# Optimization experiments

Measured on AMD Instinct MI355X. Metric: run time of the kernel, lower is better.

Reference implementation:

```python
import jax, jax.numpy as jnp
import numpy as np

C_CT, C_MRI, C_OUT = 64, 64, 64
B, D, H, W = 1, 8, 32, 32


def setup_inputs() -> dict:
    key = jax.random.key(0)
    ks = jax.random.split(key, 18)
    s = 0.05
    inp = {
        "ct_features": jax.random.normal(ks[0], (B, C_CT, D, H, W), jnp.float32),
        "mri_features": jax.random.normal(ks[1], (B, C_MRI, D, H, W), jnp.float32),
        # 1x1x1 Conv3d == per-voxel linear: weight (out, in), bias (out,)
        "wq_ct": jax.random.normal(ks[2], (C_OUT, C_CT), jnp.float32) * s,
        "bq_ct": jax.random.normal(ks[3], (C_OUT,), jnp.float32) * s,
        "wk_mri": jax.random.normal(ks[4], (C_OUT, C_MRI), jnp.float32) * s,
        "bk_mri": jax.random.normal(ks[5], (C_OUT,), jnp.float32) * s,
        "wv_mri": jax.random.normal(ks[6], (C_OUT, C_MRI), jnp.float32) * s,
        "bv_mri": jax.random.normal(ks[7], (C_OUT,), jnp.float32) * s,
        "wq_mri": jax.random.normal(ks[8], (C_OUT, C_MRI), jnp.float32) * s,
        "bq_mri": jax.random.normal(ks[9], (C_OUT,), jnp.float32) * s,
        "wk_ct": jax.random.normal(ks[10], (C_OUT, C_CT), jnp.float32) * s,
        "bk_ct": jax.random.normal(ks[11], (C_OUT,), jnp.float32) * s,
        "wv_ct": jax.random.normal(ks[12], (C_OUT, C_CT), jnp.float32) * s,
        "bv_ct": jax.random.normal(ks[13], (C_OUT,), jnp.float32) * s,
        "wo": jax.random.normal(ks[14], (C_OUT, 2 * C_OUT), jnp.float32) * s,
        "bo": jax.random.normal(ks[15], (C_OUT,), jnp.float32) * s,
    }
    return inp


def _proj(x_flat, w, b):
    # x_flat: (B, Cin, N); 1x1x1 conv -> (B, Cout, N)
    return jnp.einsum("oc,bcn->bon", w, x_flat) + b[None, :, None]


def _forward(ct, mri, wq_ct, bq_ct, wk_mri, bk_mri, wv_mri, bv_mri,
             wq_mri, bq_mri, wk_ct, bk_ct, wv_ct, bv_ct, wo, bo):
    b, _, d, h, w = ct.shape
    n = d * h * w
    ct_f = ct.reshape(b, ct.shape[1], n)
    mri_f = mri.reshape(b, mri.shape[1], n)
    scale = 1.0 / np.sqrt(C_OUT).astype(np.float32)

    # CT queries attend over MRI keys/values
    ct_q = _proj(ct_f, wq_ct, bq_ct)      # (B, C, N)
    mri_k = _proj(mri_f, wk_mri, bk_mri)  # (B, C, N)
    mri_v = _proj(mri_f, wv_mri, bv_mri)  # (B, C, N)
    attn_ct = jax.nn.softmax(jnp.einsum("bci,bcj->bij", ct_q, mri_k) * scale, axis=-1)
    ct_att = jnp.einsum("bcj,bij->bci", mri_v, attn_ct)  # (B, C, N)

    # MRI queries attend over CT keys/values
    mri_q = _proj(mri_f, wq_mri, bq_mri)
    ct_k = _proj(ct_f, wk_ct, bk_ct)
    ct_v = _proj(ct_f, wv_ct, bv_ct)
    attn_mri = jax.nn.softmax(jnp.einsum("bci,bcj->bij", mri_q, ct_k) * scale, axis=-1)
    mri_att = jnp.einsum("bcj,bij->bci", ct_v, attn_mri)

    fused = jnp.concatenate([ct_att, mri_att], axis=1)  # (B, 2C, N)
    out = _proj(fused, wo, bo)  # (B, C, N)
    return out.reshape(b, C_OUT, d, h, w)


def reference(ct_features, mri_features, wq_ct, bq_ct, wk_mri, bk_mri,
              wv_mri, bv_mri, wq_mri, bq_mri, wk_ct, bk_ct, wv_ct, bv_ct,
              wo, bo):
    return _forward(ct_features, mri_features, wq_ct, bq_ct, wk_mri, bk_mri,
                    wv_mri, bv_mri, wq_mri, bq_mri, wk_ct, bk_ct,
                    wv_ct, bv_ct, wo, bo)
```

## Files before the change

kernel.cpp:

```cpp
#include <hip/hip_runtime.h>
#include <stdint.h>

constexpr int N = 8192;
constexpr float QSCALE = 0.18033688011112042f;
constexpr int SPLIT = 4;

typedef __attribute__((ext_vector_type(4))) float f32x4;
typedef __attribute__((ext_vector_type(16))) float f32x16;
typedef __attribute__((ext_vector_type(4))) unsigned int u32x4;
typedef __attribute__((ext_vector_type(2))) unsigned int u32x2;
typedef __attribute__((ext_vector_type(4))) unsigned short u16x4;

__device__ inline unsigned short f2bf(float f) {
  unsigned u = __builtin_bit_cast(unsigned, f);
  u += 0x7FFFu + ((u >> 16) & 1u);
  return (unsigned short)(u >> 16);
}
__device__ inline float bf2f(unsigned short u) {
  return __builtin_bit_cast(float, (unsigned)u << 16);
}
__device__ inline unsigned cvtpk(float a, float b) {
  unsigned r;
  asm("v_cvt_pk_bf16_f32 %0, %1, %2" : "=v"(r) : "v"(a), "v"(b));
  return r;
}

__device__ inline void mfma32(f32x16& d, u32x4 a, u32x4 b) {
  asm volatile("v_mfma_f32_32x32x16_bf16 %0, %1, %2, %0" : "+v"(d) : "v"(a), "v"(b));
}
__device__ inline void mfma_guard() {
  __builtin_amdgcn_sched_barrier(0);
  asm volatile("s_nop 7\n\ts_nop 7");
  __builtin_amdgcn_sched_barrier(0);
}
__device__ inline void gload16(const void* src, void* lds) {
  __builtin_amdgcn_global_load_lds(
      (const __attribute__((address_space(1))) unsigned int*)src,
      (__attribute__((address_space(3))) unsigned int*)lds, 16, 0, 0);
}

struct ProjArgs {
  const float* x[6];
  const float* w[6];
  const float* b[6];
  unsigned short* o[6];
  int mode[6];
  float scale[6];
};

__global__ __launch_bounds__(256) void proj_kernel(ProjArgs A) {
  const int p = blockIdx.y;
  const float* __restrict__ x = A.x[p];
  const float* __restrict__ w = A.w[p];
  const float* __restrict__ bias = A.b[p];
  unsigned short* __restrict__ out = A.o[p];
  const int n0 = blockIdx.x * 64;
  __shared__ float Xs[64][64];
  __shared__ float Ws[64][64];
  const int t = threadIdx.x;
#pragma unroll
  for (int i = 0; i < 4; i++) {
    int s = t + i * 256;
    ((u32x4*)Ws)[s] = ((const u32x4*)w)[s];
  }
#pragma unroll
  for (int i = 0; i < 4; i++) {
    int s = t + i * 256;
    int c = s >> 4, nc = s & 15;
    *(u32x4*)&Xs[c][nc * 4] = *(const u32x4*)&x[c * N + n0 + nc * 4];
  }
  __syncthreads();
  const int n = t & 63, h = t >> 6;
  float acc[16];
#pragma unroll
  for (int o = 0; o < 16; o++) acc[o] = bias[h * 16 + o];
  for (int c = 0; c < 64; c++) {
    float xv = Xs[c][n];
#pragma unroll
    for (int o = 0; o < 16; o++) acc[o] = fmaf(Ws[h * 16 + o][c], xv, acc[o]);
  }
  const float sc = A.scale[p];
  if (A.mode[p] == 0) {
    unsigned short* po = out + (size_t)(n0 + n) * 64 + h * 16;
#pragma unroll
    for (int o = 0; o < 16; o++) po[o] = f2bf(acc[o] * sc);
  } else {
#pragma unroll
    for (int o = 0; o < 16; o++) out[(size_t)(h * 16 + o) * N + n0 + n] = f2bf(acc[o] * sc);
  }
}

__global__ __launch_bounds__(256, 2) void attn_kernel(
    const unsigned short* __restrict__ Q0, const unsigned short* __restrict__ K0,
    const unsigned short* __restrict__ V0, const unsigned short* __restrict__ Q1,
    const unsigned short* __restrict__ K1, const unsigned short* __restrict__ V1,
    unsigned short* __restrict__ Opart, float* __restrict__ Lsum) {
  const int bid = blockIdx.x;
  const int slice = bid & 7;
  const int qb = bid >> 3;
  const int dir = slice >> 2;
  const int chunk = slice & 3;
  const unsigned short* __restrict__ Q = dir ? Q1 : Q0;
  const unsigned short* __restrict__ K = dir ? K1 : K0;
  const unsigned short* __restrict__ V = dir ? V1 : V0;

  __shared__ char smem[33280];

  const int t = threadIdx.x;
  const int lane = t & 63, w = t >> 6;
  const int qsub = w >> 1, jsub = w & 1;
  const int hi = lane >> 5, l31 = lane & 31;
  const int kvbase = chunk * 2048;

  const int srowoff = lane >> 3;
  const int swzb = ((lane & 7) ^ (lane >> 3)) * 16;
  const char* const Kc = (const char*)K;
  const char* const Vc = (const char*)V;

#define STAGE(jtile, slot)                                                     \
  do {                                                                         \
    const int j0s = kvbase + (jtile) * 64;                                     \
    _Pragma("unroll") for (int i = 0; i < 2; i++) {                            \
      const int row = (w * 2 + i) * 8 + srowoff;                               \
      gload16(Kc + (size_t)(j0s + row) * 128 + swzb,                           \
              smem + (slot) * 8192 + (w * 2 + i) * 1024);                      \
      gload16(Vc + (size_t)row * (N * 2) + (size_t)j0s * 2 + swzb,             \
              smem + 16384 + (slot) * 8192 + (w * 2 + i) * 1024);              \
    }                                                                          \
  } while (0)

  u32x4 qf[2][4];
#pragma unroll
  for (int qs = 0; qs < 2; qs++) {
    const int qrow = qb * 128 + qsub * 64 + qs * 32 + l31;
#pragma unroll
    for (int ks = 0; ks < 4; ks++)
      qf[qs][ks] = *(const u32x4*)((const char*)Q + (size_t)qrow * 128 + (2 * ks + hi) * 16);
  }

  f32x16 acc[2][2];
#pragma unroll
  for (int cb = 0; cb < 2; cb++)
#pragma unroll
    for (int qs = 0; qs < 2; qs++)
#pragma unroll
      for (int r = 0; r < 16; r++) acc[cb][qs][r] = 0.f;
  float lpart[2] = {0.f, 0.f};

  STAGE(0, 0);
  for (int jt = 0; jt < 32; ++jt) {
    asm volatile("s_waitcnt vmcnt(0)" ::: "memory");
    __builtin_amdgcn_s_barrier();
    __builtin_amdgcn_sched_barrier(0);
    const int cur = jt & 1;
    if (jt + 1 < 32) STAGE(jt + 1, cur ^ 1);
    char* const Kl = smem + cur * 8192;
    char* const Vl = smem + 16384 + cur * 8192;

    u32x4 kf[4];
    {
      const int row = jsub * 32 + l31;
      const int rs = (row & 7) << 4;
#pragma unroll
      for (int ks = 0; ks < 4; ks++)
        kf[ks] = *(const u32x4*)(Kl + row * 128 + (((2 * ks + hi) * 16) ^ rs));
    }

    f32x16 st[2];
#pragma unroll
    for (int qs = 0; qs < 2; qs++)
#pragma unroll
      for (int r = 0; r < 16; r++) st[qs][r] = 0.f;
    __builtin_amdgcn_s_setprio(1);
#pragma unroll
    for (int ks = 0; ks < 4; ks++) {
      mfma32(st[0], kf[ks], qf[0][ks]);
      mfma32(st[1], kf[ks], qf[1][ks]);
    }
    __builtin_amdgcn_s_setprio(0);
    mfma_guard();

    u32x4 vf[2][2];
#pragma unroll
    for (int cb = 0; cb < 2; cb++) {
      const int row = cb * 32 + l31;
      const int rs = (row & 7) << 4;
#pragma unroll
      for (int js = 0; js < 2; js++)
        vf[cb][js] = *(const u32x4*)(Vl + row * 128 + (((jsub * 4 + js * 2 + hi) * 16) ^ rs));
    }

#pragma unroll
    for (int qs = 0; qs < 2; qs++) {
      float p[16];
#pragma unroll
      for (int r = 0; r < 16; r++) p[r] = __builtin_amdgcn_exp2f(st[qs][r]);
      lpart[qs] += (((p[0] + p[1]) + (p[2] + p[3])) + ((p[4] + p[5]) + (p[6] + p[7]))) +
                   (((p[8] + p[9]) + (p[10] + p[11])) + ((p[12] + p[13]) + (p[14] + p[15])));
      unsigned w00 = cvtpk(p[0], p[1]),   w01 = cvtpk(p[2], p[3]);
      unsigned w10 = cvtpk(p[4], p[5]),   w11 = cvtpk(p[6], p[7]);
      unsigned w20 = cvtpk(p[8], p[9]),   w21 = cvtpk(p[10], p[11]);
      unsigned w30 = cvtpk(p[12], p[13]), w31 = cvtpk(p[14], p[15]);
      asm volatile("v_permlane32_swap_b32 %0, %1" : "+v"(w00), "+v"(w10));
      asm volatile("v_permlane32_swap_b32 %0, %1" : "+v"(w01), "+v"(w11));
      asm volatile("v_permlane32_swap_b32 %0, %1" : "+v"(w20), "+v"(w30));
      asm volatile("v_permlane32_swap_b32 %0, %1" : "+v"(w21), "+v"(w31));
      u32x4 pf0, pf1;
      pf0[0] = w00; pf0[1] = w01; pf0[2] = w10; pf0[3] = w11;
      pf1[0] = w20; pf1[1] = w21; pf1[2] = w30; pf1[3] = w31;
      mfma_guard();
      __builtin_amdgcn_s_setprio(1);
      mfma32(acc[0][qs], vf[0][0], pf0);
      mfma32(acc[1][qs], vf[1][0], pf0);
      mfma32(acc[0][qs], vf[0][1], pf1);
      mfma32(acc[1][qs], vf[1][1], pf1);
      __builtin_amdgcn_s_setprio(0);
    }
  }
#undef STAGE
  mfma_guard();

#pragma unroll
  for (int qs = 0; qs < 2; qs++) lpart[qs] += __shfl_xor(lpart[qs], 32);

  __syncthreads();
  char* const obuf = smem + qsub * 16384;
  float* const mlb = (float*)(smem + 32768);
  if (jsub == 1) {
#pragma unroll
    for (int qs = 0; qs < 2; qs++) {
      const int qloc = qs * 32 + l31;
      const int qsw = (qloc & 7) << 4;
#pragma unroll
      for (int cb = 0; cb < 2; cb++)
#pragma unroll
        for (int a = 0; a < 4; a++) {
          const int ch0 = cb * 32 + 8 * a + 4 * hi;
          f32x4 v;
          v[0] = acc[cb][qs][4 * a];     v[1] = acc[cb][qs][4 * a + 1];
          v[2] = acc[cb][qs][4 * a + 2]; v[3] = acc[cb][qs][4 * a + 3];
          *(f32x4*)(obuf + qloc * 256 + ((ch0 * 4) ^ qsw)) = v;
        }
      if (hi == 0) mlb[qsub * 64 + qloc] = lpart[qs];
    }
  }
  __syncthreads();
  if (jsub == 0) {
#pragma unroll
    for (int qs = 0; qs < 2; qs++) {
      const int qloc = qs * 32 + l31;
      const int qsw = (qloc & 7) << 4;
      const int qg = qb * 128 + qsub * 64 + qloc;
      const size_t pbase = ((size_t)slice * N + qg) * 64;
#pragma unroll
      for (int cb = 0; cb < 2; cb++)
#pragma unroll
        for (int a = 0; a < 4; a++) {
          const int ch0 = cb * 32 + 8 * a + 4 * hi;
          f32x4 oo = *(const f32x4*)(obuf + qloc * 256 + ((ch0 * 4) ^ qsw));
          u32x2 pk;
          pk[0] = cvtpk(acc[cb][qs][4 * a] + oo[0], acc[cb][qs][4 * a + 1] + oo[1]);
          pk[1] = cvtpk(acc[cb][qs][4 * a + 2] + oo[2], acc[cb][qs][4 * a + 3] + oo[3]);
          *(u32x2*)(Opart + pbase + ch0) = pk;
        }
      if (hi == 0) Lsum[(size_t)slice * N + qg] = lpart[qs] + mlb[qsub * 64 + qloc];
    }
  }
}

__global__ __launch_bounds__(256) void oproj_kernel(
    const unsigned short* __restrict__ Opart, const float* __restrict__ Lsum,
    const float* __restrict__ wo, const float* __restrict__ bo,
    float* __restrict__ out) {
  __shared__ float Fs[128][32];
  __shared__ float Ws[64][128];
  const int t = threadIdx.x;
  const int n0 = blockIdx.x * 32;
#pragma unroll
  for (int i = 0; i < 8; i++) {
    int s = t + i * 256;
    ((u32x4*)Ws)[s] = ((const u32x4*)wo)[s];
  }
  const int q = t & 31;
  const int cg = t >> 5;
#pragma unroll
  for (int dir = 0; dir < 2; dir++) {
    float lt = 0.f;
#pragma unroll
    for (int c = 0; c < 4; c++) lt += Lsum[(size_t)(dir * SPLIT + c) * N + n0 + q];
    const float rD = 1.0f / lt;
#pragma unroll
    for (int i = 0; i < 2; i++) {
      const int ch4 = cg * 2 + i;
      float s0 = 0.f, s1 = 0.f, s2 = 0.f, s3 = 0.f;
#pragma unroll
      for (int c = 0; c < 4; c++) {
        u16x4 v = *(const u16x4*)(Opart +
            ((size_t)(dir * SPLIT + c) * N + n0 + q) * 64 + ch4 * 4);
        s0 += bf2f(v[0]); s1 += bf2f(v[1]); s2 += bf2f(v[2]); s3 += bf2f(v[3]);
      }
      Fs[dir * 64 + ch4 * 4 + 0][q] = s0 * rD;
      Fs[dir * 64 + ch4 * 4 + 1][q] = s1 * rD;
      Fs[dir * 64 + ch4 * 4 + 2][q] = s2 * rD;
      Fs[dir * 64 + ch4 * 4 + 3][q] = s3 * rD;
    }
  }
  __syncthreads();
  const int n = t & 31, h = t >> 5;
  float acc[8];
#pragma unroll
  for (int o = 0; o < 8; o++) acc[o] = bo[h * 8 + o];
  for (int ch = 0; ch < 128; ch++) {
    float fv = Fs[ch][n];
#pragma unroll
    for (int o = 0; o < 8; o++) acc[o] = fmaf(Ws[h * 8 + o][ch], fv, acc[o]);
  }
#pragma unroll
  for (int o = 0; o < 8; o++) out[(size_t)(h * 8 + o) * N + n0 + n] = acc[o];
}

extern "C" void kernel_launch(void* const* d_in, const int* in_sizes, int n_in,
                              void* d_out, int out_size, void* d_ws, size_t ws_size,
                              hipStream_t stream) {
  const float* ct     = (const float*)d_in[0];
  const float* mri    = (const float*)d_in[1];
  const float* wq_ct  = (const float*)d_in[2];
  const float* bq_ct  = (const float*)d_in[3];
  const float* wk_mri = (const float*)d_in[4];
  const float* bk_mri = (const float*)d_in[5];
  const float* wv_mri = (const float*)d_in[6];
  const float* bv_mri = (const float*)d_in[7];
  const float* wq_mri = (const float*)d_in[8];
  const float* bq_mri = (const float*)d_in[9];
  const float* wk_ct  = (const float*)d_in[10];
  const float* bk_ct  = (const float*)d_in[11];
  const float* wv_ct  = (const float*)d_in[12];
  const float* bv_ct  = (const float*)d_in[13];
  const float* wo     = (const float*)d_in[14];
  const float* bo     = (const float*)d_in[15];

  char* ws = (char*)d_ws;
  const size_t MB = (size_t)1 << 20;
  unsigned short* Qt_ct  = (unsigned short*)(ws + 0 * MB);
  unsigned short* Kt_mri = (unsigned short*)(ws + 1 * MB);
  unsigned short* V_mri  = (unsigned short*)(ws + 2 * MB);
  unsigned short* Qt_mri = (unsigned short*)(ws + 3 * MB);
  unsigned short* Kt_ct  = (unsigned short*)(ws + 4 * MB);
  unsigned short* V_ct   = (unsigned short*)(ws + 5 * MB);
  unsigned short* Opart  = (unsigned short*)(ws + 6 * MB);
  float* Lsum            = (float*)(ws + 14 * MB);

  ProjArgs A;
  A.x[0] = ct;  A.w[0] = wq_ct;  A.b[0] = bq_ct;  A.o[0] = Qt_ct;  A.mode[0] = 0; A.scale[0] = QSCALE;
  A.x[1] = mri; A.w[1] = wk_mri; A.b[1] = bk_mri; A.o[1] = Kt_mri; A.mode[1] = 0; A.scale[1] = 1.f;
  A.x[2] = mri; A.w[2] = wv_mri; A.b[2] = bv_mri; A.o[2] = V_mri;  A.mode[2] = 1; A.scale[2] = 1.f;
  A.x[3] = mri; A.w[3] = wq_mri; A.b[3] = bq_mri; A.o[3] = Qt_mri; A.mode[3] = 0; A.scale[3] = QSCALE;
  A.x[4] = ct;  A.w[4] = wk_ct;  A.b[4] = bk_ct;  A.o[4] = Kt_ct;  A.mode[4] = 0; A.scale[4] = 1.f;
  A.x[5] = ct;  A.w[5] = wv_ct;  A.b[5] = bv_ct;  A.o[5] = V_ct;   A.mode[5] = 1; A.scale[5] = 1.f;

  proj_kernel<<<dim3(128, 6), 256, 0, stream>>>(A);
  attn_kernel<<<dim3(512), 256, 0, stream>>>(Qt_ct, Kt_mri, V_mri,
                                             Qt_mri, Kt_ct, V_ct, Opart, Lsum);
  oproj_kernel<<<dim3(256), 256, 0, stream>>>(Opart, Lsum, wo, bo, (float*)d_out);
}
```

Before: 69.83 us.

## Give each wave a private K/V staging buffer and drop per-tile block barrier

Each wave now loads only the 32 KV rows it consumes into its own LDS region, with a new V swizzle for the narrower 64-byte rows, so the per-iteration block-wide s_barrier is removed. The prefetch is issued before waiting, and a partial vmcnt wait lets the next tile's loads stay in flight during compute. This doubles LDS use to about 66KB per block, which with launch_bounds(256,2) may limit occupancy, and the two waves sharing a query subset now load the same Q-independent K/V separately only for their own halves.

```diff
diff --git a/kernel.cpp b/kernel.cpp
--- a/kernel.cpp
+++ b/kernel.cpp
@@ -104,28 +104,31 @@
   const unsigned short* __restrict__ K = dir ? K1 : K0;
   const unsigned short* __restrict__ V = dir ? V1 : V0;
 
-  __shared__ char smem[33280];
+  __shared__ char smem[66048];
 
   const int t = threadIdx.x;
   const int lane = t & 63, w = t >> 6;
   const int qsub = w >> 1, jsub = w & 1;
   const int hi = lane >> 5, l31 = lane & 31;
   const int kvbase = chunk * 2048;
-
-  const int srowoff = lane >> 3;
-  const int swzb = ((lane & 7) ^ (lane >> 3)) * 16;
+  char* const wb = smem + w * 16384;
+
+  const int kswz = ((lane & 7) ^ (lane >> 3)) * 16;
+  const int vx = (l31 >> 3) & 3;
   const char* const Kc = (const char*)K;
   const char* const Vc = (const char*)V;
 
 #define STAGE(jtile, slot)                                                     \
   do {                                                                         \
-    const int j0s = kvbase + (jtile) * 64;                                     \
-    _Pragma("unroll") for (int i = 0; i < 2; i++) {                            \
-      const int row = (w * 2 + i) * 8 + srowoff;                               \
-      gload16(Kc + (size_t)(j0s + row) * 128 + swzb,                           \
-              smem + (slot) * 8192 + (w * 2 + i) * 1024);                      \
-      gload16(Vc + (size_t)row * (N * 2) + (size_t)j0s * 2 + swzb,             \
-              smem + 16384 + (slot) * 8192 + (w * 2 + i) * 1024);              \
+    const int j0s = kvbase + (jtile) * 64 + jsub * 32;                         \
+    _Pragma("unroll") for (int i = 0; i < 4; i++) {                            \
+      const int krow = i * 8 + (lane >> 3);                                    \
+      gload16(Kc + (size_t)(j0s + krow) * 128 + kswz,                          \
+              wb + (slot) * 8192 + i * 1024);                                  \
+      const int vrow = i * 16 + (lane >> 2);                                   \
+      gload16(Vc + (size_t)vrow * (N * 2) + (size_t)j0s * 2 +                  \
+                  (((lane & 3) ^ ((vrow >> 3) & 3)) * 16),                     \
+              wb + (slot) * 8192 + 4096 + i * 1024);                           \
     }                                                                          \
   } while (0)
 
@@ -149,21 +152,23 @@
 
   STAGE(0, 0);
   for (int jt = 0; jt < 32; ++jt) {
-    asm volatile("s_waitcnt vmcnt(0)" ::: "memory");
-    __builtin_amdgcn_s_barrier();
+    const int cur = jt & 1;
+    if (jt + 1 < 32) {
+      STAGE(jt + 1, cur ^ 1);
+      asm volatile("s_waitcnt vmcnt(8)" ::: "memory");
+    } else {
+      asm volatile("s_waitcnt vmcnt(0)" ::: "memory");
+    }
     __builtin_amdgcn_sched_barrier(0);
-    const int cur = jt & 1;
-    if (jt + 1 < 32) STAGE(jt + 1, cur ^ 1);
-    char* const Kl = smem + cur * 8192;
-    char* const Vl = smem + 16384 + cur * 8192;
+    char* const Kl = wb + cur * 8192;
+    char* const Vl = wb + cur * 8192 + 4096;
 
     u32x4 kf[4];
     {
-      const int row = jsub * 32 + l31;
-      const int rs = (row & 7) << 4;
+      const int krs = (l31 & 7) << 4;
 #pragma unroll
       for (int ks = 0; ks < 4; ks++)
-        kf[ks] = *(const u32x4*)(Kl + row * 128 + (((2 * ks + hi) * 16) ^ rs));
+        kf[ks] = *(const u32x4*)(Kl + l31 * 128 + (((2 * ks + hi) * 16) ^ krs));
     }
 
     f32x16 st[2];
@@ -184,10 +189,9 @@
 #pragma unroll
     for (int cb = 0; cb < 2; cb++) {
       const int row = cb * 32 + l31;
-      const int rs = (row & 7) << 4;
 #pragma unroll
       for (int js = 0; js < 2; js++)
-        vf[cb][js] = *(const u32x4*)(Vl + row * 128 + (((jsub * 4 + js * 2 + hi) * 16) ^ rs));
+        vf[cb][js] = *(const u32x4*)(Vl + row * 64 + (((js * 2 + hi) ^ vx) * 16));
     }
 
 #pragma unroll
@@ -225,7 +229,7 @@
 
   __syncthreads();
   char* const obuf = smem + qsub * 16384;
-  float* const mlb = (float*)(smem + 32768);
+  float* const mlb = (float*)(smem + 65536);
   if (jsub == 1) {
 #pragma unroll
     for (int qs = 0; qs < 2; qs++) {
```

After: 73.04 us. 4.6% more time.

## Triple-buffer K/V tiles and software-pipeline QK^T of next tile with softmax

Applied to the files above, without the earlier changes.

Shared-memory staging moves from double to triple buffering, so global loads are issued two tiles ahead. The loop is unrolled by two with ping-pong score registers: the QK^T MFMAs for tile j+1 are interleaved with the exp2, pack and PV MFMAs of tile j. The aim is to overlap transcendental and VALU work with matrix-core work and to hide load latency. In exchange the kernel uses more LDS (about 49KB per block) and more registers for the extra score accumulators, which may hurt occupancy under launch_bounds(256,2).

```diff
diff --git a/kernel.cpp b/kernel.cpp
--- a/kernel.cpp
+++ b/kernel.cpp
@@ -104,7 +104,7 @@
   const unsigned short* __restrict__ K = dir ? K1 : K0;
   const unsigned short* __restrict__ V = dir ? V1 : V0;
 
-  __shared__ char smem[33280];
+  __shared__ char smem[49664];
 
   const int t = threadIdx.x;
   const int lane = t & 63, w = t >> 6;
@@ -125,7 +125,7 @@
       gload16(Kc + (size_t)(j0s + row) * 128 + swzb,                           \
               smem + (slot) * 8192 + (w * 2 + i) * 1024);                      \
       gload16(Vc + (size_t)row * (N * 2) + (size_t)j0s * 2 + swzb,             \
-              smem + 16384 + (slot) * 8192 + (w * 2 + i) * 1024);              \
+              smem + 24576 + (slot) * 8192 + (w * 2 + i) * 1024);              \
     }                                                                          \
   } while (0)
 
@@ -147,76 +147,137 @@
       for (int r = 0; r < 16; r++) acc[cb][qs][r] = 0.f;
   float lpart[2] = {0.f, 0.f};
 
+#define READK(slot, kf)                                                        \
+  do {                                                                         \
+    char* const Kl_ = smem + (slot) * 8192;                                    \
+    const int row_ = jsub * 32 + l31;                                          \
+    const int rs_ = (row_ & 7) << 4;                                           \
+    _Pragma("unroll") for (int ks = 0; ks < 4; ks++)                           \
+      kf[ks] = *(const u32x4*)(Kl_ + row_ * 128 + (((2 * ks + hi) * 16) ^ rs_)); \
+  } while (0)
+
+#define ITER(jt, stO, stN)                                                     \
+  do {                                                                         \
+    asm volatile("s_waitcnt vmcnt(0)" ::: "memory");                           \
+    __builtin_amdgcn_s_barrier();                                              \
+    __builtin_amdgcn_sched_barrier(0);                                         \
+    const int sl_c = (jt) % 3;                                                 \
+    if ((jt) + 2 < 32) STAGE((jt) + 2, ((jt) + 2) % 3);                        \
+                                                       \
+    u32x4 vf[2][2];                                                            \
+    {                                                                          \
+      char* const Vl_ = smem + 24576 + sl_c * 8192;                            \
+      _Pragma("unroll") for (int cb = 0; cb < 2; cb++) {                       \
+        const int row_ = cb * 32 + l31;                                        \
+        const int rs_ = (row_ & 7) << 4;                                       \
+        _Pragma("unroll") for (int js = 0; js < 2; js++)                       \
+          vf[cb][js] = *(const u32x4*)(Vl_ + row_ * 128 +                      \
+                                       (((jsub * 4 + js * 2 + hi) * 16) ^ rs_)); \
+      }                                                                        \
+    }                                                                          \
+    u32x4 kfn[4];                                                              \
+    const bool hasNext = ((jt) + 1 < 32);                                      \
+    if (hasNext) {                                                             \
+      READK(((jt) + 1) % 3, kfn);                                              \
+      _Pragma("unroll") for (int qs = 0; qs < 2; qs++)                         \
+        _Pragma("unroll") for (int r = 0; r < 16; r++) stN[qs][r] = 0.f;       \
+      __builtin_amdgcn_s_setprio(1);                                           \
+      mfma32(stN[0], kfn[0], qf[0][0]);                                        \
+      mfma32(stN[1], kfn[0], qf[1][0]);                                        \
+      mfma32(stN[0], kfn[1], qf[0][1]);                                        \
+      mfma32(stN[1], kfn[1], qf[1][1]);                                        \
+      __builtin_amdgcn_s_setprio(0);                                           \
+    }                                                                          \
+                                 \
+    float p0[16];                                                              \
+    _Pragma("unroll") for (int r = 0; r < 16; r++)                             \
+      p0[r] = __builtin_amdgcn_exp2f(stO[0][r]);                               \
+    lpart[0] += (((p0[0]+p0[1])+(p0[2]+p0[3]))+((p0[4]+p0[5])+(p0[6]+p0[7])))  \
+              + (((p0[8]+p0[9])+(p0[10]+p0[11]))+((p0[12]+p0[13])+(p0[14]+p0[15]))); \
+    if (hasNext) {                                                             \
+      __builtin_amdgcn_s_setprio(1);                                           \
+      mfma32(stN[0], kfn[2], qf[0][2]);                                        \
+      mfma32(stN[1], kfn[2], qf[1][2]);                                        \
+      mfma32(stN[0], kfn[3], qf[0][3]);                                        \
+      mfma32(stN[1], kfn[3], qf[1][3]);                                        \
+      __builtin_amdgcn_s_setprio(0);                                           \
+    }                                                                          \
+    {                                                                          \
+      unsigned w00 = cvtpk(p0[0], p0[1]),   w01 = cvtpk(p0[2], p0[3]);         \
+      unsigned w10 = cvtpk(p0[4], p0[5]),   w11 = cvtpk(p0[6], p0[7]);         \
+      unsigned w20 = cvtpk(p0[8], p0[9]),   w21 = cvtpk(p0[10], p0[11]);       \
+      unsigned w30 = cvtpk(p0[12], p0[13]), w31 = cvtpk(p0[14], p0[15]);       \
+      asm volatile("v_permlane32_swap_b32 %0, %1" : "+v"(w00), "+v"(w10));     \
+      asm volatile("v_permlane32_swap_b32 %0, %1" : "+v"(w01), "+v"(w11));     \
+      asm volatile("v_permlane32_swap_b32 %0, %1" : "+v"(w20), "+v"(w30));     \
+      asm volatile("v_permlane32_swap_b32 %0, %1" : "+v"(w21), "+v"(w31));     \
+      u32x4 pf0, pf1;                                                          \
+      pf0[0] = w00; pf0[1] = w01; pf0[2] = w10; pf0[3] = w11;                  \
+      pf1[0] = w20; pf1[1] = w21; pf1[2] = w30; pf1[3] = w31;                  \
+      mfma_guard();                                                            \
+      __builtin_amdgcn_s_setprio(1);                                           \
+      mfma32(acc[0][0], vf[0][0], pf0);                                        \
+      mfma32(acc[1][0], vf[1][0], pf0);                                        \
+      mfma32(acc[0][0], vf[0][1], pf1);                                        \
+      mfma32(acc[1][0], vf[1][1], pf1);                                        \
+      __builtin_amdgcn_s_setprio(0);                                           \
+    }                                                                          \
+                                                                      \
+    float p1[16];                                                              \
+    _Pragma("unroll") for (int r = 0; r < 16; r++)                             \
+      p1[r] = __builtin_amdgcn_exp2f(stO[1][r]);                               \
+    lpart[1] += (((p1[0]+p1[1])+(p1[2]+p1[3]))+((p1[4]+p1[5])+(p1[6]+p1[7])))  \
+              + (((p1[8]+p1[9])+(p1[10]+p1[11]))+((p1[12]+p1[13])+(p1[14]+p1[15]))); \
+    {                                                                          \
+      unsigned w00 = cvtpk(p1[0], p1[1]),   w01 = cvtpk(p1[2], p1[3]);         \
+      unsigned w10 = cvtpk(p1[4], p1[5]),   w11 = cvtpk(p1[6], p1[7]);         \
+      unsigned w20 = cvtpk(p1[8], p1[9]),   w21 = cvtpk(p1[10], p1[11]);       \
+      unsigned w30 = cvtpk(p1[12], p1[13]), w31 = cvtpk(p1[14], p1[15]);       \
+      asm volatile("v_permlane32_swap_b32 %0, %1" : "+v"(w00), "+v"(w10));     \
+      asm volatile("v_permlane32_swap_b32 %0, %1" : "+v"(w01), "+v"(w11));     \
+      asm volatile("v_permlane32_swap_b32 %0, %1" : "+v"(w20), "+v"(w30));     \
+      asm volatile("v_permlane32_swap_b32 %0, %1" : "+v"(w21), "+v"(w31));     \
+      u32x4 pf0, pf1;                                                          \
+      pf0[0] = w00; pf0[1] = w01; pf0[2] = w10; pf0[3] = w11;                  \
+      pf1[0] = w20; pf1[1] = w21; pf1[2] = w30; pf1[3] = w31;                  \
+      mfma_guard();                                                            \
+      __builtin_amdgcn_s_setprio(1);                                           \
+      mfma32(acc[0][1], vf[0][0], pf0);                                        \
+      mfma32(acc[1][1], vf[1][0], pf0);                                        \
+      mfma32(acc[0][1], vf[0][1], pf1);                                        \
+      mfma32(acc[1][1], vf[1][1], pf1);                                        \
+      __builtin_amdgcn_s_setprio(0);                                           \
+    }                                                                          \
+  } while (0)
+
+  f32x16 stA[2], stB[2];
+
   STAGE(0, 0);
-  for (int jt = 0; jt < 32; ++jt) {
-    asm volatile("s_waitcnt vmcnt(0)" ::: "memory");
-    __builtin_amdgcn_s_barrier();
-    __builtin_amdgcn_sched_barrier(0);
-    const int cur = jt & 1;
-    if (jt + 1 < 32) STAGE(jt + 1, cur ^ 1);
-    char* const Kl = smem + cur * 8192;
-    char* const Vl = smem + 16384 + cur * 8192;
-
-    u32x4 kf[4];
-    {
-      const int row = jsub * 32 + l31;
-      const int rs = (row & 7) << 4;
-#pragma unroll
-      for (int ks = 0; ks < 4; ks++)
-        kf[ks] = *(const u32x4*)(Kl + row * 128 + (((2 * ks + hi) * 16) ^ rs));
-    }
-
-    f32x16 st[2];
+  asm volatile("s_waitcnt vmcnt(0)" ::: "memory");
+  __builtin_amdgcn_s_barrier();
+  STAGE(1, 1);
+  {
+    u32x4 kf0[4];
+    READK(0, kf0);
 #pragma unroll
     for (int qs = 0; qs < 2; qs++)
 #pragma unroll
-      for (int r = 0; r < 16; r++) st[qs][r] = 0.f;
+      for (int r = 0; r < 16; r++) stA[qs][r] = 0.f;
     __builtin_amdgcn_s_setprio(1);
 #pragma unroll
     for (int ks = 0; ks < 4; ks++) {
-      mfma32(st[0], kf[ks], qf[0][ks]);
-      mfma32(st[1], kf[ks], qf[1][ks]);
+      mfma32(stA[0], kf0[ks], qf[0][ks]);
+      mfma32(stA[1], kf0[ks], qf[1][ks]);
     }
     __builtin_amdgcn_s_setprio(0);
-    mfma_guard();
-
-    u32x4 vf[2][2];
-#pragma unroll
-    for (int cb = 0; cb < 2; cb++) {
-      const int row = cb * 32 + l31;
-      const int rs = (row & 7) << 4;
-#pragma unroll
-      for (int js = 0; js < 2; js++)
-        vf[cb][js] = *(const u32x4*)(Vl + row * 128 + (((jsub * 4 + js * 2 + hi) * 16) ^ rs));
-    }
-
-#pragma unroll
-    for (int qs = 0; qs < 2; qs++) {
-      float p[16];
-#pragma unroll
-      for (int r = 0; r < 16; r++) p[r] = __builtin_amdgcn_exp2f(st[qs][r]);
-      lpart[qs] += (((p[0] + p[1]) + (p[2] + p[3])) + ((p[4] + p[5]) + (p[6] + p[7]))) +
-                   (((p[8] + p[9]) + (p[10] + p[11])) + ((p[12] + p[13]) + (p[14] + p[15])));
-      unsigned w00 = cvtpk(p[0], p[1]),   w01 = cvtpk(p[2], p[3]);
-      unsigned w10 = cvtpk(p[4], p[5]),   w11 = cvtpk(p[6], p[7]);
-      unsigned w20 = cvtpk(p[8], p[9]),   w21 = cvtpk(p[10], p[11]);
-      unsigned w30 = cvtpk(p[12], p[13]), w31 = cvtpk(p[14], p[15]);
-      asm volatile("v_permlane32_swap_b32 %0, %1" : "+v"(w00), "+v"(w10));
-      asm volatile("v_permlane32_swap_b32 %0, %1" : "+v"(w01), "+v"(w11));
-      asm volatile("v_permlane32_swap_b32 %0, %1" : "+v"(w20), "+v"(w30));
-      asm volatile("v_permlane32_swap_b32 %0, %1" : "+v"(w21), "+v"(w31));
-      u32x4 pf0, pf1;
-      pf0[0] = w00; pf0[1] = w01; pf0[2] = w10; pf0[3] = w11;
-      pf1[0] = w20; pf1[1] = w21; pf1[2] = w30; pf1[3] = w31;
-      mfma_guard();
-      __builtin_amdgcn_s_setprio(1);
-      mfma32(acc[0][qs], vf[0][0], pf0);
-      mfma32(acc[1][qs], vf[1][0], pf0);
-      mfma32(acc[0][qs], vf[0][1], pf1);
-      mfma32(acc[1][qs], vf[1][1], pf1);
-      __builtin_amdgcn_s_setprio(0);
-    }
-  }
+  }
+
+  for (int jt = 0; jt < 32; jt += 2) {
+    ITER(jt, stA, stB);
+    ITER(jt + 1, stB, stA);
+  }
+#undef ITER
+#undef READK
 #undef STAGE
   mfma_guard();
 
@@ -225,7 +286,7 @@
 
   __syncthreads();
   char* const obuf = smem + qsub * 16384;
-  float* const mlb = (float*)(smem + 32768);
+  float* const mlb = (float*)(smem + 49152);
   if (jsub == 1) {
 #pragma unroll
     for (int qs = 0; qs < 2; qs++) {
```

Measured after the change: 70.74 us. Within noise of the previous version (+1.3%).
